# Kernel tuning notes

Measured on AMD Instinct MI355X. Metric: run time of the kernel, lower is better.

Reference implementation:

```python
import jax, jax.numpy as jnp
import numpy as np

B, S, HID, NH = 8, 1024, 1024, 16
HD = HID // NH  # 64
STR = 128
NEG = -1e10


def setup_inputs() -> dict:
    key = jax.random.key(0)
    ks = jax.random.split(key, 16)
    def lin(k, fan_in, fan_out):
        bound = 1.0 / np.sqrt(fan_in)
        kw, kb = jax.random.split(k)
        W = jax.random.uniform(kw, (fan_in, fan_out), jnp.float32, -bound, bound)
        b = jax.random.uniform(kb, (fan_out,), jnp.float32, -bound, bound)
        return W, b
    Wq, bq = lin(ks[0], HID, HID)
    Wk, bk = lin(ks[1], HID, HID)
    Wv, bv = lin(ks[2], HID, HID)
    Wsk, bsk = lin(ks[3], HID, STR)
    Wsv, bsv = lin(ks[4], HID, STR)
    Wo, bo = lin(ks[5], HID + STR, HID)
    return {
        "query": jax.random.normal(ks[6], (B, S, HID), jnp.float32),
        "key": jax.random.normal(ks[7], (B, S, HID), jnp.float32),
        "value": jax.random.normal(ks[8], (B, S, HID), jnp.float32),
        "x_rsa": jax.random.normal(ks[9], (B, S, STR), jnp.float32),
        "mask": jax.random.randint(ks[10], (B, 1, 1, S), 0, 2, jnp.int32),
        "rsa_mask": jax.random.randint(ks[11], (B, 1, 1, S), 0, 2, jnp.int32),
        "Wq": Wq, "bq": bq, "Wk": Wk, "bk": bk, "Wv": Wv, "bv": bv,
        "Wsk": Wsk, "bsk": bsk, "Wsv": Wsv, "bsv": bsv, "Wo": Wo, "bo": bo,
    }


def reference(query, key, value, x_rsa, mask, rsa_mask,
              Wq, bq, Wk, bk, Wv, bv, Wsk, bsk, Wsv, bsv, Wo, bo):
    scale = jnp.sqrt(jnp.float32(HD))
    Q = (query @ Wq + bq).reshape(B, S, NH, HD).transpose(0, 2, 1, 3)   # [B,NH,S,HD]
    K = (key @ Wk + bk).reshape(B, S, NH, HD).transpose(0, 2, 1, 3)
    V = (value @ Wv + bv).reshape(B, S, NH, HD).transpose(0, 2, 1, 3)
    str_K = (key @ Wsk + bsk)[:, None, :, :]    # [B,1,S,128]
    str_V = (value @ Wsv + bsv)[:, None, :, :]
    rsa_Q = x_rsa[:, None, :, :]                # [B,1,S,128]

    energy = jnp.einsum('bhqd,bhkd->bhqk', Q, K)           # [B,NH,S,S]
    rsa_energy = jnp.einsum('bhqd,bhkd->bhqk', rsa_Q, str_K)  # [B,1,S,S]
    # torch order: mask first, then divide by scale
    energy = jnp.where(mask == 0, NEG, energy) / scale
    rsa_energy = jnp.where(mask == 0, NEG, rsa_energy)
    rsa_energy = jnp.where(rsa_mask == 0, NEG, rsa_energy)  # str_scale == 1

    attention = jax.nn.softmax(energy, axis=-1)
    rsa_attention = jax.nn.softmax(rsa_energy, axis=-1)
    # dropout is identity in eval mode
    x = jnp.einsum('bhqk,bhkd->bhqd', attention, V)          # [B,NH,S,HD]
    rsa_x = jnp.einsum('bhqk,bhkd->bhqd', rsa_attention, str_V)  # [B,1,S,128]
    x = x.transpose(0, 2, 1, 3).reshape(B, S, HID)
    rsa_x = rsa_x.transpose(0, 2, 1, 3).reshape(B, S, STR)
    out = jnp.concatenate((x, rsa_x), axis=-1) @ Wo + bo     # [B,S,HID]
    return out, attention, rsa_attention
```

## Files before the change

### kernel.cpp

```cpp
#include <hip/hip_runtime.h>
#include <stdint.h>

typedef unsigned int u32;
typedef _Float16 f16_t;

typedef _Float16 f16x8 __attribute__((ext_vector_type(8)));
typedef __fp16   fp16x2 __attribute__((ext_vector_type(2)));
typedef float    f32x4 __attribute__((ext_vector_type(4)));

__device__ __forceinline__ f32x4 mfma16(f16x8 a, f16x8 b, f32x4 c){
  return __builtin_amdgcn_mfma_f32_16x16x32_f16(a, b, c, 0, 0, 0);
}
__device__ __forceinline__ float fexp2(float x){ return __builtin_amdgcn_exp2f(x); }
__device__ __forceinline__ u32 pkrtz(float a, float b){
  union { fp16x2 h; u32 u; } cv; cv.h = __builtin_amdgcn_cvt_pkrtz(a, b); return cv.u;
}

template<int N>
__device__ __forceinline__ void barrier_vmleave(){
  asm volatile("s_waitcnt vmcnt(%0)" :: "i"(N) : "memory");
  __builtin_amdgcn_s_barrier();
}

__device__ __forceinline__ void gl_lds16(const void* g, void* l){
  typedef const __attribute__((address_space(1))) void* gasp;
  typedef __attribute__((address_space(3))) void* lasp;
  gasp gp = reinterpret_cast<gasp>(reinterpret_cast<uintptr_t>(g));
  lasp lp = reinterpret_cast<lasp>(static_cast<u32>(reinterpret_cast<uintptr_t>(l)));
  __builtin_amdgcn_global_load_lds(gp, lp, 16, 0, 0);
}

template<int NBYTES, int ROWB, int NT>
__device__ __forceinline__ void stage_swz(const char* gbase, u32 gstrideB, char* lds, int tid){
  const u32 lane = (u32)(tid & 63);
  #pragma unroll
  for (int j = 0; j < NBYTES/(NT*16); ++j){
    u32 o   = (u32)(j*NT + tid) * 16u;
    u32 row = o / (u32)ROWB;
    u32 col = (o % (u32)ROWB) ^ ((row & ((u32)(ROWB>>4)-1u)) << 4);
    gl_lds16(gbase + (size_t)row * gstrideB + col, lds + (o - lane*16u));
  }
}

template<int ROWB>
__device__ __forceinline__ u32 swzb(u32 row, u32 col){
  return col ^ ((row & ((u32)(ROWB>>4)-1u)) << 4);
}

template<int ROWB>
__device__ __forceinline__ f16x8 frag_ld(const char* lds, u32 row, u32 kbyte){
  return *reinterpret_cast<const f16x8*>(lds + (size_t)row*ROWB + swzb<ROWB>(row, kbyte));
}

__device__ __forceinline__ void cvt8(const float* __restrict__ in, f16_t* __restrict__ out, u32 i){
  const f32x4* p = reinterpret_cast<const f32x4*>(in) + 2*(size_t)i;
  f32x4 a = p[0], b = p[1];
  f16x8 v;
  v[0]=(f16_t)a[0]; v[1]=(f16_t)a[1]; v[2]=(f16_t)a[2]; v[3]=(f16_t)a[3];
  v[4]=(f16_t)b[0]; v[5]=(f16_t)b[1]; v[6]=(f16_t)b[2]; v[7]=(f16_t)b[3];
  *(reinterpret_cast<f16x8*>(out) + i) = v;
}

__global__ void prep_all(const float* __restrict__ q, const float* __restrict__ k,
                         const float* __restrict__ v, const float* __restrict__ xr,
                         const int* __restrict__ mask, const int* __restrict__ rmask,
                         f16_t* __restrict__ qo, f16_t* __restrict__ ko,
                         f16_t* __restrict__ vo, f16_t* __restrict__ xo,
                         float* __restrict__ mb, float* __restrict__ rb,
                         const float* __restrict__ Wq, const float* __restrict__ Wk,
                         const float* __restrict__ Wv, const float* __restrict__ Wsk,
                         const float* __restrict__ Wsv, const float* __restrict__ Wo,
                         f16_t* __restrict__ wqT, f16_t* __restrict__ wkT, f16_t* __restrict__ wvT,
                         f16_t* __restrict__ wskT, f16_t* __restrict__ wsvT, f16_t* __restrict__ woT)
{
  __shared__ float tile[32][33];
  u32 b = blockIdx.x;
  if (b < 12288u){
    const float* in; f16_t* out; u32 base;
    if (b < 4096u){ in=q; out=qo; base=0u; }
    else if (b < 8192u){ in=k; out=ko; base=4096u; }
    else { in=v; out=vo; base=8192u; }
    cvt8(in, out, (b-base)*256u + threadIdx.x);
  } else if (b < 12800u){
    cvt8(xr, xo, (b-12288u)*256u + threadIdx.x);
  } else if (b < 12832u){
    u32 i = (b-12800u)*256u + threadIdx.x;
    int m = mask[i]; int r = rmask[i];
    mb[i] = m ? 0.0f : -1.0e9f;
    rb[i] = (m && r) ? 0.0f : -1.0e9f;
  } else {
    u32 t = b - 12832u;
    const float* W; f16_t* WT; u32 K, N, i, j;
    if (t < 3072u){
      u32 w = t >> 10, l = t & 1023u;
      W = w==0 ? Wq : w==1 ? Wk : Wv;
      WT = w==0 ? wqT : w==1 ? wkT : wvT;
      K = 1024u; N = 1024u; i = l & 31u; j = l >> 5;
    } else if (t < 3328u){
      u32 l = t - 3072u;
      W  = l < 128u ? Wsk : Wsv;
      WT = l < 128u ? wskT : wsvT;
      l &= 127u;
      K = 1024u; N = 128u; i = l & 31u; j = l >> 5;
    } else {
      u32 l = t - 3328u;
      W = Wo; WT = woT; K = 1152u; N = 1024u; i = l % 36u; j = l / 36u;
    }
    const u32 k0 = i*32u, n0 = j*32u;
    const int tt = threadIdx.x;
    const int r = tt >> 3, c4 = (tt & 7) * 4;
    f32x4 val = *reinterpret_cast<const f32x4*>(W + (size_t)(k0 + r)*N + n0 + c4);
    tile[r][c4+0]=val[0]; tile[r][c4+1]=val[1]; tile[r][c4+2]=val[2]; tile[r][c4+3]=val[3];
    __syncthreads();
    union { f16_t x[4]; uint64_t u; } pk;
    #pragma unroll
    for (int jj=0;jj<4;++jj) pk.x[jj] = (f16_t)tile[c4+jj][r];
    *reinterpret_cast<uint64_t*>(WT + (size_t)(n0 + r)*K + k0 + c4) = pk.u;
  }
}

struct GArg { const f16_t* A; const f16_t* Bt; const float* bias; void* C; u32 lda, ldb, ldc, K; int mode; };
struct GPack { GArg g[5]; int single; };

__global__ __launch_bounds__(256, 2)
void gemm_bt(GPack p)
{
  __shared__ char As[2][16384];
  __shared__ char Bs[2][16384];
  GArg g; u32 bn;
  const u32 bm = blockIdx.y * 128u;
  if (p.single >= 0){ g = p.g[p.single]; bn = blockIdx.x*128u; }
  else if (blockIdx.z == 0u){ if (blockIdx.x >= 2u) return; g = p.g[3u+blockIdx.x]; bn = 0u; }
  else { g = p.g[blockIdx.z-1u]; bn = blockIdx.x*128u; }

  const int tid = threadIdx.x, lane = tid & 63, wid = tid >> 6;
  const int wr = wid >> 1, wc = wid & 1;
  const char* Ab = (const char*)(g.A + (size_t)bm * g.lda);
  const char* Bb = (const char*)(g.Bt + (size_t)bn * g.ldb);
  const u32 ldaB = g.lda*2u, ldbB = g.ldb*2u;
  const bool swp = (g.mode != 2);

  f32x4 acc[4][4] = {};
  const int nt = (int)(g.K >> 6);

  stage_swz<16384,128,256>(Ab, ldaB, As[0], tid);
  stage_swz<16384,128,256>(Bb, ldbB, Bs[0], tid);
  __syncthreads();

  for (int t = 0; t < nt; ++t){
    if (t + 1 < nt){
      stage_swz<16384,128,256>(Ab + (size_t)(t+1)*128, ldaB, As[(t+1)&1], tid);
      stage_swz<16384,128,256>(Bb + (size_t)(t+1)*128, ldbB, Bs[(t+1)&1], tid);
    }
    const char* as = As[t&1]; const char* bs = Bs[t&1];
    f16x8 af[4][2], bf[4][2];
    #pragma unroll
    for (int mi=0; mi<4; ++mi)
      #pragma unroll
      for (int ks=0; ks<2; ++ks)
        af[mi][ks] = frag_ld<128>(as, (u32)(wr*64 + mi*16 + (lane&15)), (u32)(ks*64 + ((lane>>4)<<4)));
    #pragma unroll
    for (int ni=0; ni<4; ++ni)
      #pragma unroll
      for (int ks=0; ks<2; ++ks)
        bf[ni][ks] = frag_ld<128>(bs, (u32)(wc*64 + ni*16 + (lane&15)), (u32)(ks*64 + ((lane>>4)<<4)));
    __builtin_amdgcn_s_setprio(1);
    if (swp){
      #pragma unroll
      for (int mi=0; mi<4; ++mi)
        #pragma unroll
        for (int ni=0; ni<4; ++ni)
          #pragma unroll
          for (int ks=0; ks<2; ++ks)
            acc[mi][ni] = mfma16(bf[ni][ks], af[mi][ks], acc[mi][ni]);
    } else {
      #pragma unroll
      for (int mi=0; mi<4; ++mi)
        #pragma unroll
        for (int ni=0; ni<4; ++ni)
          #pragma unroll
          for (int ks=0; ks<2; ++ks)
            acc[mi][ni] = mfma16(af[mi][ks], bf[ni][ks], acc[mi][ni]);
    }
    __builtin_amdgcn_s_setprio(0);
    __syncthreads();
  }

  if (g.mode == 2){
    float bv[4];
    #pragma unroll
    for (int ni=0; ni<4; ++ni) bv[ni] = g.bias[bn + wc*64 + ni*16 + (lane&15)];
    f16_t* C = (f16_t*)g.C;
    #pragma unroll
    for (int mi=0; mi<4; ++mi){
      #pragma unroll
      for (int ni=0; ni<4; ++ni){
        u32 n  = bn + (u32)(wc*64 + ni*16 + (lane&15));
        u32 m0 = bm + (u32)(wr*64 + mi*16 + ((lane>>4)<<2));
        size_t idx0 = ((size_t)(m0>>10)*g.ldc + n)*1024 + (m0 & 1023);
        union { f16_t v[4]; uint64_t u; } pk;
        #pragma unroll
        for (int r=0;r<4;++r) pk.v[r] = (f16_t)(acc[mi][ni][r] + bv[ni]);
        *reinterpret_cast<uint64_t*>(C + idx0) = pk.u;
      }
    }
  } else {
    f32x4 bf4[4];
    #pragma unroll
    for (int ni=0; ni<4; ++ni)
      bf4[ni] = *reinterpret_cast<const f32x4*>(g.bias + bn + wc*64 + ni*16 + ((lane>>4)<<2));
    #pragma unroll
    for (int mi=0; mi<4; ++mi){
      u32 m = bm + (u32)(wr*64 + mi*16 + (lane&15));
      #pragma unroll
      for (int ni=0; ni<4; ++ni){
        u32 n0 = bn + (u32)(wc*64 + ni*16 + ((lane>>4)<<2));
        if (g.mode == 0){
          float* C = (float*)g.C;
          f32x4 v = acc[mi][ni] + bf4[ni];
          *reinterpret_cast<f32x4*>(C + (size_t)m*g.ldc + n0) = v;
        } else if (g.mode == 1){
          f16_t* C = (f16_t*)g.C;
          size_t idx = (((size_t)(m>>10)*16 + (n0>>6))*1024 + (m&1023))*64 + (n0&63);
          union { f16_t v[4]; uint64_t u; } pk;
          #pragma unroll
          for (int r=0;r<4;++r) pk.v[r] = (f16_t)(acc[mi][ni][r] + bf4[ni][r]);
          *reinterpret_cast<uint64_t*>(C + idx) = pk.u;
        } else {
          f16_t* C = (f16_t*)g.C;
          union { f16_t v[4]; uint64_t u; } pk;
          #pragma unroll
          for (int r=0;r<4;++r) pk.v[r] = (f16_t)(acc[mi][ni][r] + bf4[ni][r]);
          *reinterpret_cast<uint64_t*>(C + (size_t)m*g.ldc + n0) = pk.u;
        }
      }
    }
  }
}

template<int D, int KCH, int KCH1, int BSHIFT, int SCALEBIT>
__device__ __forceinline__ void attn_fused_body(char* smem,
    const f16_t* __restrict__ Qg, const f16_t* __restrict__ Kg, const f16_t* __restrict__ Vtg,
    const float* __restrict__ mbias,
    float* __restrict__ attnOut, f16_t* __restrict__ xout, u32 xld, u32 xcolAdd,
    const int tid, const u32 qt, const u32 batch)
{
  constexpr int S = 1024;
  constexpr int ROWB  = D*2;
  constexpr int ROWBV = KCH*2;
  constexpr int MI   = KCH/16;
  constexpr int MI1  = KCH1/16;
  constexpr int KSL  = D/32;
  constexpr int PSL  = KCH/32;
  constexpr int MIPV = D/16;
  char* Qs  = smem;
  char* Ks0 = Qs + 128*ROWB;
  char* Ks1 = Ks0 + KCH*ROWB;
  char* Vs0 = Ks1 + KCH*ROWB;
  char* Vs1 = Vs0 + D*ROWBV;
  char* L1K0 = Qs + 128*ROWB;
  char* L1K1 = L1K0 + KCH1*ROWB;

  const int lane = tid & 63, wq = tid >> 6;
  const int ql = lane & 15, h = lane >> 4;
  const u32 bb = batch >> BSHIFT;
  const float scale = SCALEBIT ? 0.1803368801111244f : 1.4426950408889634f;
  const f16_t* qb = Qg + ((size_t)batch*S + (size_t)qt*128)*D;
  const f16_t* kb = Kg + (size_t)batch*S*D;
  const char* vtb = (const char*)(Vtg + (size_t)batch*D*S);
  const float* mbb = mbias + (size_t)bb*S;

  const u32 q = qt*128u + (u32)(wq*16 + ql);
  const u32 qrow = (u32)(wq*16 + ql);
  float* arow = attnOut + (size_t)batch*S*S + (size_t)q*S;

  stage_swz<128*ROWB, ROWB, 512>((const char*)qb, ROWB, Qs, tid);
  stage_swz<KCH1*ROWB, ROWB, 512>((const char*)kb, ROWB, L1K0, tid);
  __syncthreads();

  float sacc = 0.0f;
  constexpr int NCH1 = S / KCH1;
  for (int ch = 0; ch < NCH1; ++ch){
    if (ch + 1 < NCH1)
      stage_swz<KCH1*ROWB, ROWB, 512>((const char*)(kb + (size_t)(ch+1)*KCH1*D), ROWB, ((ch+1)&1)?L1K1:L1K0, tid);
    const char* ks = (ch&1) ? L1K1 : L1K0;

    f32x4 acc[MI1] = {};
    __builtin_amdgcn_s_setprio(1);
    #pragma unroll
    for (int ksl=0; ksl<KSL; ++ksl){
      f16x8 bf = frag_ld<ROWB>(Qs, qrow, (u32)(ksl*64 + h*16));
      #pragma unroll
      for (int mi=0; mi<MI1; ++mi){
        f16x8 af = frag_ld<ROWB>(ks, (u32)(mi*16 + ql), (u32)(ksl*64 + h*16));
        acc[mi] = mfma16(af, bf, acc[mi]);
      }
    }
    __builtin_amdgcn_s_setprio(0);
    #pragma unroll
    for (int mi=0; mi<MI1; ++mi){
      f32x4 mb = *reinterpret_cast<const f32x4*>(mbb + ch*KCH1 + mi*16 + h*4);
      #pragma unroll
      for (int r=0;r<4;++r) sacc += fexp2(acc[mi][r]*scale + mb[r]);
    }
    __syncthreads();
  }

  sacc += __shfl_xor(sacc, 16);
  sacc += __shfl_xor(sacc, 32);
  const float rreg = 1.0f / sacc;

  f32x4 accX[MIPV] = {};
  stage_swz<KCH*ROWB, ROWB, 512>((const char*)kb, ROWB, Ks0, tid);
  stage_swz<D*ROWBV, ROWBV, 512>(vtb, (u32)(S*2), Vs0, tid);
  __syncthreads();

  const int bidx = ((ql | ((h & 1) << 5)) << 2);

  constexpr int NCH = S / KCH;
  for (int ch = 0; ch < NCH; ++ch){
    if (ch + 1 < NCH){
      stage_swz<KCH*ROWB, ROWB, 512>((const char*)(kb + (size_t)(ch+1)*KCH*D), ROWB, ((ch+1)&1)?Ks1:Ks0, tid);
      stage_swz<D*ROWBV, ROWBV, 512>(vtb + (size_t)(ch+1)*KCH*2, (u32)(S*2), ((ch+1)&1)?Vs1:Vs0, tid);
    }
    const char* ks = (ch&1) ? Ks1 : Ks0;
    const char* vs = (ch&1) ? Vs1 : Vs0;

    f32x4 acc[MI] = {};
    __builtin_amdgcn_s_setprio(1);
    #pragma unroll
    for (int ksl=0; ksl<KSL; ++ksl){
      f16x8 bf = frag_ld<ROWB>(Qs, qrow, (u32)(ksl*64 + h*16));
      #pragma unroll
      for (int mi=0; mi<MI; ++mi){
        f16x8 af = frag_ld<ROWB>(ks, (u32)(mi*16 + ql), (u32)(ksl*64 + h*16));
        acc[mi] = mfma16(af, bf, acc[mi]);
      }
    }
    __builtin_amdgcn_s_setprio(0);

    u32 pk[MI][2];
    #pragma unroll
    for (int mi=0; mi<MI; ++mi){
      f32x4 mb = *reinterpret_cast<const f32x4*>(mbb + ch*KCH + mi*16 + h*4);
      f32x4 pv;
      #pragma unroll
      for (int r=0;r<4;++r)
        pv[r] = fexp2(acc[mi][r]*scale + mb[r]) * rreg;
      *reinterpret_cast<f32x4*>(arow + ch*KCH + mi*16 + h*4) = pv;
      pk[mi][0] = pkrtz(pv[0], pv[1]);
      pk[mi][1] = pkrtz(pv[2], pv[3]);
    }

    #pragma unroll
    for (int psl=0; psl<PSL; ++psl){
      union { u32 w[4]; f16x8 v; } pb;
      #pragma unroll
      for (int s=0; s<4; ++s){
        int ii = bidx + ((s & 2) ? 64 : 0);
        u32 pa  = (u32)__builtin_amdgcn_ds_bpermute(ii, (int)pk[2*psl][s&1]);
        u32 pbv = (u32)__builtin_amdgcn_ds_bpermute(ii, (int)pk[2*psl+1][s&1]);
        pb.w[s] = (lane & 32) ? pbv : pa;
      }
      __builtin_amdgcn_s_setprio(1);
      #pragma unroll
      for (int mi2=0; mi2<MIPV; ++mi2){
        f16x8 vf = frag_ld<ROWBV>(vs, (u32)(mi2*16 + ql), (u32)(psl*64 + h*16));
        accX[mi2] = mfma16(vf, pb.v, accX[mi2]);
      }
      __builtin_amdgcn_s_setprio(0);
    }

    barrier_vmleave<MI>();
  }

  u32 col0 = (batch & ((1u<<BSHIFT)-1u)) * (u32)D + xcolAdd;
  #pragma unroll
  for (int mi2=0; mi2<MIPV; ++mi2){
    union { f16_t v[4]; uint64_t u; } pk4;
    #pragma unroll
    for (int r=0;r<4;++r) pk4.v[r] = (f16_t)accX[mi2][r];
    *reinterpret_cast<uint64_t*>(xout + ((size_t)bb*S + q)*xld + col0 + mi2*16 + h*4) = pk4.u;
  }
}

__global__ __launch_bounds__(512, 4)
void attn_all(const f16_t* __restrict__ Qh, const f16_t* __restrict__ Kh,
              const f16_t* __restrict__ Vth, const float* __restrict__ mbias,
              float* __restrict__ attnp,
              const f16_t* __restrict__ xrf, const f16_t* __restrict__ strK,
              const f16_t* __restrict__ strVt, const float* __restrict__ rbias,
              float* __restrict__ rsap,
              f16_t* __restrict__ conc)
{
  __shared__ char smem[65536];
  const int tid = threadIdx.x;
  const u32 qt = blockIdx.y & 7u;
  const u32 bh = blockIdx.x * 17u + (blockIdx.y >> 3);
  if (bh < 8u) attn_fused_body<128,32,64,0,0>(smem, xrf, strK, strVt, rbias, rsap, conc, 1152u, 1024u, tid, qt, bh);
  else         attn_fused_body<64, 64,128,4,1>(smem, Qh,  Kh,   Vth,   mbias, attnp, conc, 1152u, 0u,    tid, qt, bh-8u);
}

extern "C" void kernel_launch(void* const* d_in, const int* in_sizes, int n_in,
                              void* d_out, int out_size, void* d_ws, size_t ws_size,
                              hipStream_t stream)
{
  const float* query = (const float*)d_in[0];
  const float* key   = (const float*)d_in[1];
  const float* value = (const float*)d_in[2];
  const float* x_rsa = (const float*)d_in[3];
  const int*   mask  = (const int*)d_in[4];
  const int*   rmask = (const int*)d_in[5];
  const float* Wq = (const float*)d_in[6];  const float* bq = (const float*)d_in[7];
  const float* Wk = (const float*)d_in[8];  const float* bk = (const float*)d_in[9];
  const float* Wv = (const float*)d_in[10]; const float* bv = (const float*)d_in[11];
  const float* Wsk= (const float*)d_in[12]; const float* bsk= (const float*)d_in[13];
  const float* Wsv= (const float*)d_in[14]; const float* bsv= (const float*)d_in[15];
  const float* Wo = (const float*)d_in[16]; const float* bo = (const float*)d_in[17];

  char* ws = (char*)d_ws;
  size_t off = 0;
  auto alloc = [&](size_t bytes)->char*{ char* p = ws + off; off += (bytes + 255) & ~(size_t)255; return p; };

  f16_t* q16  = (f16_t*)alloc(16777216);
  f16_t* k16  = (f16_t*)alloc(16777216);
  f16_t* v16  = (f16_t*)alloc(16777216);
  f16_t* xrf  = (f16_t*)alloc(2097152);
  f16_t* wqT  = (f16_t*)alloc(2097152);
  f16_t* wkT  = (f16_t*)alloc(2097152);
  f16_t* wvT  = (f16_t*)alloc(2097152);
  f16_t* wskT = (f16_t*)alloc(262144);
  f16_t* wsvT = (f16_t*)alloc(262144);
  f16_t* woT  = (f16_t*)alloc(2359296);
  f16_t* Qh   = (f16_t*)alloc(16777216);
  f16_t* Kh   = (f16_t*)alloc(16777216);
  f16_t* Vth  = (f16_t*)alloc(16777216);
  f16_t* strK = (f16_t*)alloc(2097152);
  f16_t* strVt= (f16_t*)alloc(2097152);
  f16_t* conc = (f16_t*)alloc(18874368);
  float* mbias= (float*)alloc(32768);
  float* rbias= (float*)alloc(32768);

  prep_all<<<17312,256,0,stream>>>(query, key, value, x_rsa, mask, rmask,
                                   q16, k16, v16, xrf, mbias, rbias,
                                   Wq, Wk, Wv, Wsk, Wsv, Wo,
                                   wqT, wkT, wvT, wskT, wsvT, woT);

  {
    GPack pm{};
    pm.g[0] = {q16, wqT,  bq,  (void*)Qh,    1024u,1024u,0u,   1024u, 1};
    pm.g[1] = {k16, wkT,  bk,  (void*)Kh,    1024u,1024u,0u,   1024u, 1};
    pm.g[2] = {v16, wvT,  bv,  (void*)Vth,   1024u,1024u,1024u,1024u, 2};
    pm.g[3] = {k16, wskT, bsk, (void*)strK,  1024u,1024u,128u, 1024u, 3};
    pm.g[4] = {v16, wsvT, bsv, (void*)strVt, 1024u,1024u,128u, 1024u, 2};
    pm.single = -1;
    gemm_bt<<<dim3(8,64,4),256,0,stream>>>(pm);
  }

  float* outp  = (float*)d_out;
  float* attnp = outp + 8388608;
  float* rsap  = outp + 8388608 + 134217728;

  attn_all<<<dim3(8,136),512,0,stream>>>(Qh, Kh, Vth, mbias, attnp,
                                         xrf, strK, strVt, rbias, rsap, conc);

  {
    GPack po{};
    po.g[0] = {conc, woT, bo, (void*)outp, 1152u,1152u,1024u,1152u, 0};
    po.g[1] = po.g[0]; po.g[2] = po.g[0]; po.g[3] = po.g[0]; po.g[4] = po.g[0];
    po.single = 0;
    gemm_bt<<<dim3(8,64,1),256,0,stream>>>(po);
  }

  (void)in_sizes; (void)n_in; (void)out_size; (void)ws_size;
}
```

Baseline: 405.7 us.

## Make main-head attention single-pass by stashing unnormalized probabilities in registers

```diff
diff --git a/kernel.cpp b/kernel.cpp
--- a/kernel.cpp
+++ b/kernel.cpp
@@ -164,7 +164,6 @@
       #pragma unroll
       for (int ks=0; ks<2; ++ks)
         bf[ni][ks] = frag_ld<128>(bs, (u32)(wc*64 + ni*16 + (lane&15)), (u32)(ks*64 + ((lane>>4)<<4)));
-    __builtin_amdgcn_s_setprio(1);
     if (swp){
       #pragma unroll
       for (int mi=0; mi<4; ++mi)
@@ -182,7 +181,6 @@
           for (int ks=0; ks<2; ++ks)
             acc[mi][ni] = mfma16(af[mi][ks], bf[ni][ks], acc[mi][ni]);
     }
-    __builtin_amdgcn_s_setprio(0);
     __syncthreads();
   }
 
@@ -238,8 +236,138 @@
   }
 }
 
+template<int D, int KCH, int BSHIFT, int SCALEBIT>
+__device__ __forceinline__ void attn_single_body(char* smem,
+    const f16_t* __restrict__ Qg, const f16_t* __restrict__ Kg, const f16_t* __restrict__ Vtg,
+    const float* __restrict__ mbias,
+    float* __restrict__ attnOut, f16_t* __restrict__ xout, u32 xld, u32 xcolAdd,
+    const int tid, const u32 qt, const u32 batch)
+{
+  constexpr int S = 1024;
+  constexpr int ROWB  = D*2;
+  constexpr int ROWBV = KCH*2;
+  constexpr int MI   = KCH/16;
+  constexpr int KSL  = D/32;
+  constexpr int PSL  = KCH/32;
+  constexpr int MIPV = D/16;
+  constexpr int NCH  = S / KCH;
+  char* Qs  = smem;
+  char* Ks0 = Qs + 128*ROWB;
+  char* Ks1 = Ks0 + KCH*ROWB;
+  char* Vs0 = Ks1 + KCH*ROWB;
+  char* Vs1 = Vs0 + D*ROWBV;
+
+  const int lane = tid & 63, wq = tid >> 6;
+  const int ql = lane & 15, h = lane >> 4;
+  const u32 bb = batch >> BSHIFT;
+  const float scale = SCALEBIT ? 0.1803368801111244f : 1.4426950408889634f;
+  const f16_t* qb = Qg + ((size_t)batch*S + (size_t)qt*128)*D;
+  const f16_t* kb = Kg + (size_t)batch*S*D;
+  const char* vtb = (const char*)(Vtg + (size_t)batch*D*S);
+  const float* mbb = mbias + (size_t)bb*S;
+
+  const u32 q = qt*128u + (u32)(wq*16 + ql);
+  const u32 qrow = (u32)(wq*16 + ql);
+  float* arow = attnOut + (size_t)batch*S*S + (size_t)q*S;
+
+  stage_swz<128*ROWB, ROWB, 512>((const char*)qb, ROWB, Qs, tid);
+  stage_swz<KCH*ROWB, ROWB, 512>((const char*)kb, ROWB, Ks0, tid);
+  stage_swz<D*ROWBV, ROWBV, 512>(vtb, (u32)(S*2), Vs0, tid);
+  __syncthreads();
+
+  const int bidx = ((ql | ((h & 1) << 5)) << 2);
+
+  u32 stash[NCH*MI*2];
+  float sacc = 0.0f;
+  f32x4 accX[MIPV] = {};
+
+  #pragma unroll
+  for (int ch = 0; ch < NCH; ++ch){
+    if (ch + 1 < NCH){
+      stage_swz<KCH*ROWB, ROWB, 512>((const char*)(kb + (size_t)(ch+1)*KCH*D), ROWB, ((ch+1)&1)?Ks1:Ks0, tid);
+      stage_swz<D*ROWBV, ROWBV, 512>(vtb + (size_t)(ch+1)*KCH*2, (u32)(S*2), ((ch+1)&1)?Vs1:Vs0, tid);
+    }
+    const char* ks = (ch&1) ? Ks1 : Ks0;
+    const char* vs = (ch&1) ? Vs1 : Vs0;
+
+    f32x4 acc[MI] = {};
+    #pragma unroll
+    for (int ksl=0; ksl<KSL; ++ksl){
+      f16x8 bf = frag_ld<ROWB>(Qs, qrow, (u32)(ksl*64 + h*16));
+      #pragma unroll
+      for (int mi=0; mi<MI; ++mi){
+        f16x8 af = frag_ld<ROWB>(ks, (u32)(mi*16 + ql), (u32)(ksl*64 + h*16));
+        acc[mi] = mfma16(af, bf, acc[mi]);
+      }
+    }
+
+    #pragma unroll
+    for (int mi=0; mi<MI; ++mi){
+      f32x4 mb = *reinterpret_cast<const f32x4*>(mbb + ch*KCH + mi*16 + h*4);
+      float p0 = fexp2(acc[mi][0]*scale + mb[0]);
+      float p1 = fexp2(acc[mi][1]*scale + mb[1]);
+      float p2 = fexp2(acc[mi][2]*scale + mb[2]);
+      float p3 = fexp2(acc[mi][3]*scale + mb[3]);
+      sacc += (p0 + p1) + (p2 + p3);
+      stash[(ch*MI + mi)*2 + 0] = pkrtz(p0, p1);
+      stash[(ch*MI + mi)*2 + 1] = pkrtz(p2, p3);
+    }
+
+    #pragma unroll
+    for (int psl=0; psl<PSL; ++psl){
+      union { u32 w[4]; f16x8 v; } pb;
+      #pragma unroll
+      for (int s=0; s<4; ++s){
+        int ii = bidx + ((s & 2) ? 64 : 0);
+        u32 pa  = (u32)__builtin_amdgcn_ds_bpermute(ii, (int)stash[(ch*MI + 2*psl)*2 + (s&1)]);
+        u32 pbv = (u32)__builtin_amdgcn_ds_bpermute(ii, (int)stash[(ch*MI + 2*psl+1)*2 + (s&1)]);
+        pb.w[s] = (lane & 32) ? pbv : pa;
+      }
+      #pragma unroll
+      for (int mi2=0; mi2<MIPV; ++mi2){
+        f16x8 vf = frag_ld<ROWBV>(vs, (u32)(mi2*16 + ql), (u32)(psl*64 + h*16));
+        accX[mi2] = mfma16(vf, pb.v, accX[mi2]);
+      }
+    }
+
+    if (ch + 1 < NCH){
+      asm volatile("s_waitcnt vmcnt(0)" ::: "memory");
+      __builtin_amdgcn_s_barrier();
+    }
+  }
+
+  sacc += __shfl_xor(sacc, 16);
+  sacc += __shfl_xor(sacc, 32);
+  const float rreg = 1.0f / sacc;
+
+  #pragma unroll
+  for (int ch = 0; ch < NCH; ++ch){
+    #pragma unroll
+    for (int mi=0; mi<MI; ++mi){
+      union { fp16x2 h; u32 u; } a, b;
+      a.u = stash[(ch*MI + mi)*2 + 0];
+      b.u = stash[(ch*MI + mi)*2 + 1];
+      f32x4 pv;
+      pv[0] = (float)a.h[0] * rreg;
+      pv[1] = (float)a.h[1] * rreg;
+      pv[2] = (float)b.h[0] * rreg;
+      pv[3] = (float)b.h[1] * rreg;
+      *reinterpret_cast<f32x4*>(arow + ch*KCH + mi*16 + h*4) = pv;
+    }
+  }
+
+  u32 col0 = (batch & ((1u<<BSHIFT)-1u)) * (u32)D + xcolAdd;
+  #pragma unroll
+  for (int mi2=0; mi2<MIPV; ++mi2){
+    union { f16_t v[4]; uint64_t u; } pk4;
+    #pragma unroll
+    for (int r=0;r<4;++r) pk4.v[r] = (f16_t)(accX[mi2][r] * rreg);
+    *reinterpret_cast<uint64_t*>(xout + ((size_t)bb*S + q)*xld + col0 + mi2*16 + h*4) = pk4.u;
+  }
+}
+
 template<int D, int KCH, int KCH1, int BSHIFT, int SCALEBIT>
-__device__ __forceinline__ void attn_fused_body(char* smem,
+__device__ __forceinline__ void attn_twopass_body(char* smem,
     const f16_t* __restrict__ Qg, const f16_t* __restrict__ Kg, const f16_t* __restrict__ Vtg,
     const float* __restrict__ mbias,
     float* __restrict__ attnOut, f16_t* __restrict__ xout, u32 xld, u32 xcolAdd,
@@ -286,7 +414,6 @@
     const char* ks = (ch&1) ? L1K1 : L1K0;
 
     f32x4 acc[MI1] = {};
-    __builtin_amdgcn_s_setprio(1);
     #pragma unroll
     for (int ksl=0; ksl<KSL; ++ksl){
       f16x8 bf = frag_ld<ROWB>(Qs, qrow, (u32)(ksl*64 + h*16));
@@ -296,7 +423,6 @@
         acc[mi] = mfma16(af, bf, acc[mi]);
       }
     }
-    __builtin_amdgcn_s_setprio(0);
     #pragma unroll
     for (int mi=0; mi<MI1; ++mi){
       f32x4 mb = *reinterpret_cast<const f32x4*>(mbb + ch*KCH1 + mi*16 + h*4);
@@ -327,7 +453,6 @@
     const char* vs = (ch&1) ? Vs1 : Vs0;
 
     f32x4 acc[MI] = {};
-    __builtin_amdgcn_s_setprio(1);
     #pragma unroll
     for (int ksl=0; ksl<KSL; ++ksl){
       f16x8 bf = frag_ld<ROWB>(Qs, qrow, (u32)(ksl*64 + h*16));
@@ -337,7 +462,6 @@
         acc[mi] = mfma16(af, bf, acc[mi]);
       }
     }
-    __builtin_amdgcn_s_setprio(0);
 
     u32 pk[MI][2];
     #pragma unroll
@@ -362,13 +486,11 @@
         u32 pbv = (u32)__builtin_amdgcn_ds_bpermute(ii, (int)pk[2*psl+1][s&1]);
         pb.w[s] = (lane & 32) ? pbv : pa;
       }
-      __builtin_amdgcn_s_setprio(1);
       #pragma unroll
       for (int mi2=0; mi2<MIPV; ++mi2){
         f16x8 vf = frag_ld<ROWBV>(vs, (u32)(mi2*16 + ql), (u32)(psl*64 + h*16));
         accX[mi2] = mfma16(vf, pb.v, accX[mi2]);
       }
-      __builtin_amdgcn_s_setprio(0);
     }
 
     barrier_vmleave<MI>();
@@ -384,7 +506,7 @@
   }
 }
 
-__global__ __launch_bounds__(512, 4)
+__global__ __launch_bounds__(512, 2)
 void attn_all(const f16_t* __restrict__ Qh, const f16_t* __restrict__ Kh,
               const f16_t* __restrict__ Vth, const float* __restrict__ mbias,
               float* __restrict__ attnp,
@@ -397,8 +519,8 @@
   const int tid = threadIdx.x;
   const u32 qt = blockIdx.y & 7u;
   const u32 bh = blockIdx.x * 17u + (blockIdx.y >> 3);
-  if (bh < 8u) attn_fused_body<128,32,64,0,0>(smem, xrf, strK, strVt, rbias, rsap, conc, 1152u, 1024u, tid, qt, bh);
-  else         attn_fused_body<64, 64,128,4,1>(smem, Qh,  Kh,   Vth,   mbias, attnp, conc, 1152u, 0u,    tid, qt, bh-8u);
+  if (bh < 8u) attn_twopass_body<128,32,64,0,0>(smem, xrf, strK, strVt, rbias, rsap, conc, 1152u, 1024u, tid, qt, bh);
+  else         attn_single_body<64, 64,4,1>(smem, Qh, Kh, Vth, mbias, attnp, conc, 1152u, 0u, tid, qt, bh-8u);
 }
 
 extern "C" void kernel_launch(void* const* d_in, const int* in_sizes, int n_in,
```

New measurement: 553.3 us. +36.4%, slower.

## Shrink attention blocks to 64 queries, hold Q fragments in registers

Applied to the files above, without the earlier changes.

```diff
diff --git a/kernel.cpp b/kernel.cpp
--- a/kernel.cpp
+++ b/kernel.cpp
@@ -164,7 +164,6 @@
       #pragma unroll
       for (int ks=0; ks<2; ++ks)
         bf[ni][ks] = frag_ld<128>(bs, (u32)(wc*64 + ni*16 + (lane&15)), (u32)(ks*64 + ((lane>>4)<<4)));
-    __builtin_amdgcn_s_setprio(1);
     if (swp){
       #pragma unroll
       for (int mi=0; mi<4; ++mi)
@@ -182,7 +181,6 @@
           for (int ks=0; ks<2; ++ks)
             acc[mi][ni] = mfma16(af[mi][ks], bf[ni][ks], acc[mi][ni]);
     }
-    __builtin_amdgcn_s_setprio(0);
     __syncthreads();
   }
 
@@ -239,7 +237,7 @@
 }
 
 template<int D, int KCH, int KCH1, int BSHIFT, int SCALEBIT>
-__device__ __forceinline__ void attn_fused_body(char* smem,
+__device__ __forceinline__ void attn_body(char* smem,
     const f16_t* __restrict__ Qg, const f16_t* __restrict__ Kg, const f16_t* __restrict__ Vtg,
     const float* __restrict__ mbias,
     float* __restrict__ attnOut, f16_t* __restrict__ xout, u32 xld, u32 xcolAdd,
@@ -253,50 +251,48 @@
   constexpr int KSL  = D/32;
   constexpr int PSL  = KCH/32;
   constexpr int MIPV = D/16;
-  char* Qs  = smem;
-  char* Ks0 = Qs + 128*ROWB;
-  char* Ks1 = Ks0 + KCH*ROWB;
-  char* Vs0 = Ks1 + KCH*ROWB;
-  char* Vs1 = Vs0 + D*ROWBV;
-  char* L1K0 = Qs + 128*ROWB;
-  char* L1K1 = L1K0 + KCH1*ROWB;
 
   const int lane = tid & 63, wq = tid >> 6;
   const int ql = lane & 15, h = lane >> 4;
   const u32 bb = batch >> BSHIFT;
   const float scale = SCALEBIT ? 0.1803368801111244f : 1.4426950408889634f;
-  const f16_t* qb = Qg + ((size_t)batch*S + (size_t)qt*128)*D;
+  const f16_t* qb = Qg + ((size_t)batch*S + (size_t)qt*64)*D;
   const f16_t* kb = Kg + (size_t)batch*S*D;
   const char* vtb = (const char*)(Vtg + (size_t)batch*D*S);
   const float* mbb = mbias + (size_t)bb*S;
 
-  const u32 q = qt*128u + (u32)(wq*16 + ql);
   const u32 qrow = (u32)(wq*16 + ql);
+  const u32 q = qt*64u + qrow;
   float* arow = attnOut + (size_t)batch*S*S + (size_t)q*S;
 
-  stage_swz<128*ROWB, ROWB, 512>((const char*)qb, ROWB, Qs, tid);
-  stage_swz<KCH1*ROWB, ROWB, 512>((const char*)kb, ROWB, L1K0, tid);
+  stage_swz<64*ROWB, ROWB, 256>((const char*)qb, ROWB, smem, tid);
+  __syncthreads();
+  f16x8 qf[KSL];
+  #pragma unroll
+  for (int ksl=0; ksl<KSL; ++ksl)
+    qf[ksl] = frag_ld<ROWB>(smem, qrow, (u32)(ksl*64 + h*16));
+  __syncthreads();
+
+  char* L1K0 = smem;
+  char* L1K1 = smem + KCH1*ROWB;
+  stage_swz<KCH1*ROWB, ROWB, 256>((const char*)kb, ROWB, L1K0, tid);
   __syncthreads();
 
   float sacc = 0.0f;
   constexpr int NCH1 = S / KCH1;
   for (int ch = 0; ch < NCH1; ++ch){
     if (ch + 1 < NCH1)
-      stage_swz<KCH1*ROWB, ROWB, 512>((const char*)(kb + (size_t)(ch+1)*KCH1*D), ROWB, ((ch+1)&1)?L1K1:L1K0, tid);
+      stage_swz<KCH1*ROWB, ROWB, 256>((const char*)(kb + (size_t)(ch+1)*KCH1*D), ROWB, ((ch+1)&1)?L1K1:L1K0, tid);
     const char* ks = (ch&1) ? L1K1 : L1K0;
 
     f32x4 acc[MI1] = {};
-    __builtin_amdgcn_s_setprio(1);
-    #pragma unroll
-    for (int ksl=0; ksl<KSL; ++ksl){
-      f16x8 bf = frag_ld<ROWB>(Qs, qrow, (u32)(ksl*64 + h*16));
+    #pragma unroll
+    for (int ksl=0; ksl<KSL; ++ksl)
       #pragma unroll
       for (int mi=0; mi<MI1; ++mi){
         f16x8 af = frag_ld<ROWB>(ks, (u32)(mi*16 + ql), (u32)(ksl*64 + h*16));
-        acc[mi] = mfma16(af, bf, acc[mi]);
-      }
-    }
-    __builtin_amdgcn_s_setprio(0);
+        acc[mi] = mfma16(af, qf[ksl], acc[mi]);
+      }
     #pragma unroll
     for (int mi=0; mi<MI1; ++mi){
       f32x4 mb = *reinterpret_cast<const f32x4*>(mbb + ch*KCH1 + mi*16 + h*4);
@@ -310,9 +306,13 @@
   sacc += __shfl_xor(sacc, 32);
   const float rreg = 1.0f / sacc;
 
+  char* Ks0 = smem;
+  char* Ks1 = Ks0 + KCH*ROWB;
+  char* Vs0 = Ks1 + KCH*ROWB;
+  char* Vs1 = Vs0 + D*ROWBV;
   f32x4 accX[MIPV] = {};
-  stage_swz<KCH*ROWB, ROWB, 512>((const char*)kb, ROWB, Ks0, tid);
-  stage_swz<D*ROWBV, ROWBV, 512>(vtb, (u32)(S*2), Vs0, tid);
+  stage_swz<KCH*ROWB, ROWB, 256>((const char*)kb, ROWB, Ks0, tid);
+  stage_swz<D*ROWBV, ROWBV, 256>(vtb, (u32)(S*2), Vs0, tid);
   __syncthreads();
 
   const int bidx = ((ql | ((h & 1) << 5)) << 2);
@@ -320,24 +320,20 @@
   constexpr int NCH = S / KCH;
   for (int ch = 0; ch < NCH; ++ch){
     if (ch + 1 < NCH){
-      stage_swz<KCH*ROWB, ROWB, 512>((const char*)(kb + (size_t)(ch+1)*KCH*D), ROWB, ((ch+1)&1)?Ks1:Ks0, tid);
-      stage_swz<D*ROWBV, ROWBV, 512>(vtb + (size_t)(ch+1)*KCH*2, (u32)(S*2), ((ch+1)&1)?Vs1:Vs0, tid);
+      stage_swz<KCH*ROWB, ROWB, 256>((const char*)(kb + (size_t)(ch+1)*KCH*D), ROWB, ((ch+1)&1)?Ks1:Ks0, tid);
+      stage_swz<D*ROWBV, ROWBV, 256>(vtb + (size_t)(ch+1)*KCH*2, (u32)(S*2), ((ch+1)&1)?Vs1:Vs0, tid);
     }
     const char* ks = (ch&1) ? Ks1 : Ks0;
     const char* vs = (ch&1) ? Vs1 : Vs0;
 
     f32x4 acc[MI] = {};
-    __builtin_amdgcn_s_setprio(1);
-    #pragma unroll
-    for (int ksl=0; ksl<KSL; ++ksl){
-      f16x8 bf = frag_ld<ROWB>(Qs, qrow, (u32)(ksl*64 + h*16));
+    #pragma unroll
+    for (int ksl=0; ksl<KSL; ++ksl)
       #pragma unroll
       for (int mi=0; mi<MI; ++mi){
         f16x8 af = frag_ld<ROWB>(ks, (u32)(mi*16 + ql), (u32)(ksl*64 + h*16));
-        acc[mi] = mfma16(af, bf, acc[mi]);
-      }
-    }
-    __builtin_amdgcn_s_setprio(0);
+        acc[mi] = mfma16(af, qf[ksl], acc[mi]);
+      }
 
     u32 pk[MI][2];
     #pragma unroll
@@ -362,13 +358,11 @@
         u32 pbv = (u32)__builtin_amdgcn_ds_bpermute(ii, (int)pk[2*psl+1][s&1]);
         pb.w[s] = (lane & 32) ? pbv : pa;
       }
-      __builtin_amdgcn_s_setprio(1);
       #pragma unroll
       for (int mi2=0; mi2<MIPV; ++mi2){
         f16x8 vf = frag_ld<ROWBV>(vs, (u32)(mi2*16 + ql), (u32)(psl*64 + h*16));
         accX[mi2] = mfma16(vf, pb.v, accX[mi2]);
       }
-      __builtin_amdgcn_s_setprio(0);
     }
 
     barrier_vmleave<MI>();
@@ -384,7 +378,7 @@
   }
 }
 
-__global__ __launch_bounds__(512, 4)
+__global__ __launch_bounds__(256, 4)
 void attn_all(const f16_t* __restrict__ Qh, const f16_t* __restrict__ Kh,
               const f16_t* __restrict__ Vth, const float* __restrict__ mbias,
               float* __restrict__ attnp,
@@ -393,12 +387,12 @@
               float* __restrict__ rsap,
               f16_t* __restrict__ conc)
 {
-  __shared__ char smem[65536];
+  __shared__ char smem[32768];
   const int tid = threadIdx.x;
-  const u32 qt = blockIdx.y & 7u;
-  const u32 bh = blockIdx.x * 17u + (blockIdx.y >> 3);
-  if (bh < 8u) attn_fused_body<128,32,64,0,0>(smem, xrf, strK, strVt, rbias, rsap, conc, 1152u, 1024u, tid, qt, bh);
-  else         attn_fused_body<64, 64,128,4,1>(smem, Qh,  Kh,   Vth,   mbias, attnp, conc, 1152u, 0u,    tid, qt, bh-8u);
+  const u32 qt = blockIdx.y & 15u;
+  const u32 bh = blockIdx.x * 17u + (blockIdx.y >> 4);
+  if (bh < 8u) attn_body<128,32,64,0,0>(smem, xrf, strK, strVt, rbias, rsap, conc, 1152u, 1024u, tid, qt, bh);
+  else         attn_body<64, 64,128,4,1>(smem, Qh,  Kh,   Vth,   mbias, attnp, conc, 1152u, 0u,    tid, qt, bh-8u);
 }
 
 extern "C" void kernel_launch(void* const* d_in, const int* in_sizes, int n_in,
@@ -461,7 +455,7 @@
   float* attnp = outp + 8388608;
   float* rsap  = outp + 8388608 + 134217728;
 
-  attn_all<<<dim3(8,136),512,0,stream>>>(Qh, Kh, Vth, mbias, attnp,
+  attn_all<<<dim3(8,272),256,0,stream>>>(Qh, Kh, Vth, mbias, attnp,
                                          xrf, strK, strVt, rbias, rsap, conc);
 
   {
```

New measurement: 402.4 us. Within noise of the previous version (-0.8%).
